# Optimization experiments

Measured on AMD Instinct MI355X. Metric: run time of the kernel, lower is better.

The kernel has to match this reference:

```python
import jax, jax.numpy as jnp
import numpy as np

NUM_NODE = 50000
NUM_EDGE = 1_600_000
NUM_REL = 512
DIM = 64


def setup_inputs() -> dict:
    key = jax.random.key(0)
    k1, k2, k3, k4, k5, k6 = jax.random.split(key, 6)
    inp = jax.random.normal(k1, (NUM_NODE, DIM), dtype=jnp.float32)
    boundary = jax.random.normal(k2, (NUM_NODE, DIM), dtype=jnp.float32)
    node_in = jax.random.randint(k3, (NUM_EDGE,), 0, NUM_NODE)
    node_out = jax.random.randint(k4, (NUM_EDGE,), 0, NUM_NODE)
    rel = jax.random.randint(k5, (NUM_EDGE,), 0, NUM_REL)
    edge_list = jnp.stack([node_in, node_out, rel], axis=1).astype(jnp.int32)
    edge_weight = jnp.ones((NUM_EDGE,), dtype=jnp.float32)
    relation_weight = jax.random.normal(k6, (NUM_REL, DIM), dtype=jnp.float32)
    W = jax.random.normal(jax.random.fold_in(key, 7), (DIM, DIM), dtype=jnp.float32) / np.sqrt(DIM)
    b = jnp.zeros((DIM,), dtype=jnp.float32)
    return {"input": inp, "boundary": boundary, "edge_list": edge_list,
            "edge_weight": edge_weight, "relation_weight": relation_weight,
            "W": W, "b": b}


def reference(input, boundary, edge_list, edge_weight, relation_weight, W, b):
    node_in = edge_list[:, 0]
    node_out = edge_list[:, 1]
    rel = edge_list[:, 2]
    # message: DistMult = x_src * r_e   [E, D]
    msg = input[node_in] * relation_weight[rel]
    msg = msg * edge_weight[:, None]
    # std aggregation: sum and sq_sum scatters, boundary acts as an extra self-message
    s = jax.ops.segment_sum(msg, node_out, num_segments=NUM_NODE) + boundary
    sq = jax.ops.segment_sum(msg * msg, node_out, num_segments=NUM_NODE) + boundary * boundary
    deg = jax.ops.segment_sum(jnp.ones_like(edge_weight), node_out, num_segments=NUM_NODE)
    deg1 = (deg + 1.0)[:, None]  # degree_out + 1 (boundary counted)
    update = jnp.sqrt(jnp.clip(sq / deg1 - (s / deg1) ** 2, 1e-6))
    # add_model: single Linear (MLP with num_mlp_layer=1, no trailing activation)
    return update @ W.T + b
```

## Files before the change

### kernel.cpp

```cpp
#include <hip/hip_runtime.h>
#include <hip/hip_bf16.h>

#define NN  50000
#define NE  1600000
#define DIM 64
#define NBK 391

#define OFF_FLAGS  0
#define OFF_BCURP  8
#define OFF_EIDX   6272

#define CHUNK 8192
#define QCAP  2304

typedef __bf16 bf16x8 __attribute__((ext_vector_type(8)));
typedef __bf16 bf16x4 __attribute__((ext_vector_type(4)));
typedef float  f32x4  __attribute__((ext_vector_type(4)));

__device__ __forceinline__ float loadF(const void* p, int i, int bf) {
  if (bf) return __bfloat162float(((const __hip_bfloat16*)p)[i]);
  return ((const float*)p)[i];
}

__device__ __forceinline__ float4 loadF4(const void* p, int i4, int bf) {
  if (bf) {
    ushort4 u = ((const ushort4*)p)[i4];
    float4 f;
    union { unsigned int ui; float fl; } c;
    c.ui = (unsigned int)u.x << 16; f.x = c.fl;
    c.ui = (unsigned int)u.y << 16; f.y = c.fl;
    c.ui = (unsigned int)u.z << 16; f.z = c.fl;
    c.ui = (unsigned int)u.w << 16; f.w = c.fl;
    return f;
  }
  return ((const float4*)p)[i4];
}

__device__ __forceinline__ void accumF(float4 a, float4 r,
                                       float4& s4, float4& q4) {
  float tx = a.x * r.x, ty = a.y * r.y, tz = a.z * r.z, tw = a.w * r.w;
  s4.x += tx; q4.x = fmaf(tx, tx, q4.x);
  s4.y += ty; q4.y = fmaf(ty, ty, q4.y);
  s4.z += tz; q4.z = fmaf(tz, tz, q4.z);
  s4.w += tw; q4.w = fmaf(tw, tw, q4.w);
}

__global__ void k_detect(const void* input, const void* boundary,
                         const void* relw, const void* W, const void* ew,
                         int* flags, int* bcurp) {
  __shared__ int cnt;
  int t = threadIdx.x;
  const void* arrs[4] = {input, boundary, relw, W};
  for (int a = 0; a < 4; ++a) {
    if (t == 0) cnt = 0;
    __syncthreads();
    const unsigned short* u = (const unsigned short*)arrs[a];
    unsigned ex = (u[2 * t] >> 7) & 0xFF;
    if (ex >= 100 && ex <= 140) atomicAdd(&cnt, 1);
    __syncthreads();
    if (t == 0) flags[a] = (cnt >= 32) ? 1 : 0;
    __syncthreads();
  }
  if (t == 0) {
    flags[4] = (((const unsigned short*)ew)[0] == 0x3F80) ? 1 : 0;
    flags[5] = 1;
  }
  for (int i = t; i < NBK * 16; i += 64) bcurp[i] = 0;
}

__global__ __launch_bounds__(256) void k_ew(const void* __restrict__ ew,
                                            int* __restrict__ flags) {
  int bfE = flags[4];
  int c0 = blockIdx.x * 8192;
  int bad = 0;
  for (int i = threadIdx.x; i < 8192; i += 256) {
    int e = c0 + i;
    if (e < NE && loadF(ew, e, bfE) != 1.0f) bad = 1;
  }
  if (bad) flags[5] = 0;
}

__global__ __launch_bounds__(1024) void k_parta(
    const int* __restrict__ el, int* __restrict__ bcurp,
    int* __restrict__ eidx, const int* __restrict__ flags,
    int gb0, int gb1, int padcap) {
  __shared__ int stage[CHUNK];
  __shared__ unsigned short sbk[CHUNK];
  __shared__ int lh[NBK], lbase[NBK], lh2[NBK], gbs[NBK];
  __shared__ int sc[256];
  __shared__ int total;
  int t = threadIdx.x;
  int nb = gb1 - gb0;
  int c0 = blockIdx.x * CHUNK;
  int ones = flags[5];
  for (int i = t; i < nb; i += 1024) { lh[i] = 0; lh2[i] = 0; }
  __syncthreads();

  int rec[8], bb[8];
  #pragma unroll
  for (int j = 0; j < 8; ++j) {
    int e = c0 + j * 1024 + t;
    bb[j] = -1; rec[j] = 0;
    if (e < NE) {
      int n0 = el[e * 3], n1 = el[e * 3 + 1], n2 = el[e * 3 + 2];
      int b = (n1 >> 7) - gb0;
      if (b >= 0 && b < nb) {
        bb[j] = b;
        rec[j] = ones ? (n0 | (n2 << 16) | ((n1 & 127) << 25))
                      : (e | ((n1 & 127) << 25));
        atomicAdd(&lh[b], 1);
      }
    }
  }
  __syncthreads();

  int a0 = 0, a1 = 0;
  if (t < 256) {
    a0 = (2 * t < nb) ? lh[2 * t] : 0;
    a1 = (2 * t + 1 < nb) ? lh[2 * t + 1] : 0;
    sc[t] = a0 + a1;
  }
  __syncthreads();
  for (int off = 1; off < 256; off <<= 1) {
    int v = 0;
    if (t < 256 && t >= off) v = sc[t - off];
    __syncthreads();
    if (t < 256) sc[t] += v;
    __syncthreads();
  }
  if (t < 256) {
    int excl = sc[t] - (a0 + a1);
    if (2 * t < nb) {
      lbase[2 * t] = excl;
      if (a0 > 0) gbs[2 * t] = atomicAdd(&bcurp[(gb0 + 2 * t) * 16], a0);
    }
    if (2 * t + 1 < nb) {
      lbase[2 * t + 1] = excl + a0;
      if (a1 > 0)
        gbs[2 * t + 1] = atomicAdd(&bcurp[(gb0 + 2 * t + 1) * 16], a1);
    }
    if (t == 255) total = sc[255];
  }
  __syncthreads();

  #pragma unroll
  for (int j = 0; j < 8; ++j) {
    if (bb[j] >= 0) {
      int r = atomicAdd(&lh2[bb[j]], 1);
      int slot = lbase[bb[j]] + r;
      stage[slot] = rec[j];
      sbk[slot] = (unsigned short)bb[j];
    }
  }
  __syncthreads();

  int tot = total;
  for (int i = t; i < tot; i += 1024) {
    int b = sbk[i];
    int slot = gbs[b] + (i - lbase[b]);
    if (slot < padcap) eidx[(long)b * padcap + slot] = stage[i];
  }
}

__global__ __launch_bounds__(256, 8) void k_node(
    const void* __restrict__ input, const void* __restrict__ boundary,
    const int* __restrict__ el, const void* __restrict__ ew,
    const void* __restrict__ relw, const void* __restrict__ W,
    const void* __restrict__ bv, const int* __restrict__ bcurp,
    const int* __restrict__ eidx, const int* __restrict__ flags,
    void* __restrict__ out, int gb0, int hi, int padcap) {
  __shared__ int ld[QCAP];
  __shared__ int ld2[QCAP];
  __shared__ int lstart[32], lend[32], lcnt[32];
  __shared__ int nf, ovf;
  __bf16 (*updb)[72] = reinterpret_cast<__bf16(*)[72]>(ld);

  int bfI = flags[0], bfB = flags[1], bfR = flags[2], bfW = flags[3],
      bfE = flags[4], ones = flags[5];
  int t = threadIdx.x;
  int wv = t >> 6, ln = t & 63;
  int g = ln >> 4;
  int k = ln & 15;
  int q = ln >> 4;
  int Bl = blockIdx.x >> 2;
  int B  = gb0 + Bl;
  int quarter = blockIdx.x & 3;
  int n0 = B * 128 + quarter * 32;
  int cnt = bcurp[B * 16];
  const int* myeidx = eidx + (long)Bl * padcap;

  if (t == 0) { nf = 0; ovf = (cnt > padcap) ? 1 : 0; }
  if (t < 32) lcnt[t] = 0;
  __syncthreads();

  int cl = cnt < padcap ? cnt : padcap;
  for (int i = t; i < cl; i += 256) {
    int rc = myeidx[i];
    if ((((unsigned)rc) >> 30) == (unsigned)quarter) {
      int p = atomicAdd(&nf, 1);
      if (p < QCAP) ld[p] = rc; else ovf = 1;
    }
  }
  __syncthreads();
  int fast = !ovf;
  int nq = nf < QCAP ? nf : QCAP;

  if (fast) {
    for (int i = t; i < nq; i += 256)
      atomicAdd(&lcnt[(((unsigned)ld[i]) >> 25) & 31], 1);
  }
  __syncthreads();
  if (t < 32) lend[t] = lcnt[t];
  __syncthreads();
  for (int off = 1; off < 32; off <<= 1) {
    int v = 0;
    if (t < 32 && t >= off) v = lend[t - off];
    __syncthreads();
    if (t < 32) lend[t] += v;
    __syncthreads();
  }
  if (t < 32) { lstart[t] = lend[t] - lcnt[t]; lcnt[t] = 0; }
  __syncthreads();
  if (fast) {
    for (int i = t; i < nq; i += 256) {
      int rc = ld[i];
      int l = (((unsigned)rc) >> 25) & 31;
      int r = atomicAdd(&lcnt[l], 1);
      ld2[lstart[l] + r] = rc;
    }
  }
  __syncthreads();

  const float4* inp4 = (const float4*)input;
  const float4* rw4  = (const float4*)relw;
  int hot = (!bfI && !bfR && ones) ? 1 : 0;

  for (int rr = 0; rr < 8; ++rr) {
    int row = wv * 8 + rr;
    int n = n0 + row;
    if (n >= hi) {
      if (g == 0) *(bf16x4*)&updb[row][4 * k] =
          bf16x4{(__bf16)0.f, (__bf16)0.f, (__bf16)0.f, (__bf16)0.f};
      continue;
    }
    float4 s4 = {0.f,0.f,0.f,0.f}, q4 = {0.f,0.f,0.f,0.f};
    float degf = 0.f;
    if (fast) {
      int start = lstart[row], end = lend[row];
      degf = (float)(end - start);
      if (hot) {
        for (int base = start; base < end; base += 64) {
          int mm = end - base; if (mm > 64) mm = 64;
          int rec = 0;
          if (ln < mm) rec = ld2[base + ln];
          int jq = mm >> 2;
          int jmax = (mm + 3) >> 2;
          int j = 0;
          for (; j + 4 <= jq; j += 4) {
            int pk0 = __shfl(rec, j * 4 + g);
            int pk1 = __shfl(rec, j * 4 + 4 + g);
            int pk2 = __shfl(rec, j * 4 + 8 + g);
            int pk3 = __shfl(rec, j * 4 + 12 + g);
            float4 a0 = inp4[(pk0 & 0xFFFF) * 16 + k];
            float4 r0 = rw4[((pk0 >> 16) & 0x1FF) * 16 + k];
            float4 a1 = inp4[(pk1 & 0xFFFF) * 16 + k];
            float4 r1 = rw4[((pk1 >> 16) & 0x1FF) * 16 + k];
            float4 a2 = inp4[(pk2 & 0xFFFF) * 16 + k];
            float4 r2 = rw4[((pk2 >> 16) & 0x1FF) * 16 + k];
            float4 a3 = inp4[(pk3 & 0xFFFF) * 16 + k];
            float4 r3 = rw4[((pk3 >> 16) & 0x1FF) * 16 + k];
            accumF(a0, r0, s4, q4);
            accumF(a1, r1, s4, q4);
            accumF(a2, r2, s4, q4);
            accumF(a3, r3, s4, q4);
          }
          for (; j < jq; ++j) {
            int pk = __shfl(rec, j * 4 + g);
            float4 a = inp4[(pk & 0xFFFF) * 16 + k];
            float4 r = rw4[((pk >> 16) & 0x1FF) * 16 + k];
            accumF(a, r, s4, q4);
          }
          for (; j < jmax; ++j) {
            int slot = j * 4 + g;
            int pk = __shfl(rec, slot & 63);
            float wsel = (slot < mm) ? 1.0f : 0.0f;
            float4 a = inp4[(pk & 0xFFFF) * 16 + k];
            float4 r = rw4[((pk >> 16) & 0x1FF) * 16 + k];
            float tx = a.x*r.x, ty = a.y*r.y, tz = a.z*r.z, tw = a.w*r.w;
            s4.x = fmaf(wsel, tx, s4.x); q4.x = fmaf(wsel*tx, tx, q4.x);
            s4.y = fmaf(wsel, ty, s4.y); q4.y = fmaf(wsel*ty, ty, q4.y);
            s4.z = fmaf(wsel, tz, s4.z); q4.z = fmaf(wsel*tz, tz, q4.z);
            s4.w = fmaf(wsel, tw, s4.w); q4.w = fmaf(wsel*tw, tw, q4.w);
          }
        }
      } else {
        for (int base = start; base < end; base += 64) {
          int mm = end - base; if (mm > 64) mm = 64;
          int rec = 0; float wrec = 0.0f;
          if (ln < mm) {
            rec = ld2[base + ln] & 0x1FFFFFF;
            if (!ones) wrec = loadF(ew, rec, bfE);
          }
          int jmax = (mm + 3) >> 2;
          for (int j = 0; j < jmax; ++j) {
            int slot = j * 4 + g;
            int rj = __shfl(rec, slot);
            int nin, rl; float wj;
            if (ones) { nin = rj & 0xFFFF; rl = (rj >> 16) & 0x1FF; wj = 1.0f; }
            else      { nin = el[rj * 3]; rl = el[rj * 3 + 2];
                        wj = __shfl(wrec, slot); }
            float wsel = (slot < mm) ? wj : 0.0f;
            float4 a = loadF4(input, nin * 16 + k, bfI);
            float4 r = loadF4(relw, rl * 16 + k, bfR);
            float tx = a.x*r.x, ty = a.y*r.y, tz = a.z*r.z, tw = a.w*r.w;
            s4.x = fmaf(wsel, tx, s4.x); q4.x = fmaf(wsel*tx, tx, q4.x);
            s4.y = fmaf(wsel, ty, s4.y); q4.y = fmaf(wsel*ty, ty, q4.y);
            s4.z = fmaf(wsel, tz, s4.z); q4.z = fmaf(wsel*tz, tz, q4.z);
            s4.w = fmaf(wsel, tw, s4.w); q4.w = fmaf(wsel*tw, tw, q4.w);
          }
        }
      }
    } else {
      float degc = 0.f;
      for (int e0 = g; e0 < NE; e0 += 4) {
        int nout = el[e0 * 3 + 1];
        if (nout != n) continue;
        degc += 1.0f;
        int nin = el[e0 * 3], rl = el[e0 * 3 + 2];
        float wj = ones ? 1.0f : loadF(ew, e0, bfE);
        float4 a = loadF4(input, nin * 16 + k, bfI);
        float4 r = loadF4(relw, rl * 16 + k, bfR);
        float tx = wj*a.x*r.x, ty = wj*a.y*r.y, tz = wj*a.z*r.z,
              tw = wj*a.w*r.w;
        s4.x += tx; q4.x = fmaf(tx, tx, q4.x);
        s4.y += ty; q4.y = fmaf(ty, ty, q4.y);
        s4.z += tz; q4.z = fmaf(tz, tz, q4.z);
        s4.w += tw; q4.w = fmaf(tw, tw, q4.w);
      }
      degc += __shfl_xor(degc, 16); degc += __shfl_xor(degc, 32);
      degf = degc;
    }
    s4.x += __shfl_xor(s4.x, 16); s4.x += __shfl_xor(s4.x, 32);
    s4.y += __shfl_xor(s4.y, 16); s4.y += __shfl_xor(s4.y, 32);
    s4.z += __shfl_xor(s4.z, 16); s4.z += __shfl_xor(s4.z, 32);
    s4.w += __shfl_xor(s4.w, 16); s4.w += __shfl_xor(s4.w, 32);
    q4.x += __shfl_xor(q4.x, 16); q4.x += __shfl_xor(q4.x, 32);
    q4.y += __shfl_xor(q4.y, 16); q4.y += __shfl_xor(q4.y, 32);
    q4.z += __shfl_xor(q4.z, 16); q4.z += __shfl_xor(q4.z, 32);
    q4.w += __shfl_xor(q4.w, 16); q4.w += __shfl_xor(q4.w, 32);
    if (g == 0) {
      float4 b4 = loadF4(boundary, n * 16 + k, bfB);
      float dg = degf + 1.0f;
      float sv, qv;
      bf16x4 u;
      sv = (s4.x + b4.x) / dg; qv = (q4.x + b4.x * b4.x) / dg;
      u[0] = (__bf16)sqrtf(fmaxf(qv - sv * sv, 1e-6f));
      sv = (s4.y + b4.y) / dg; qv = (q4.y + b4.y * b4.y) / dg;
      u[1] = (__bf16)sqrtf(fmaxf(qv - sv * sv, 1e-6f));
      sv = (s4.z + b4.z) / dg; qv = (q4.z + b4.z * b4.z) / dg;
      u[2] = (__bf16)sqrtf(fmaxf(qv - sv * sv, 1e-6f));
      sv = (s4.w + b4.w) / dg; qv = (q4.w + b4.w * b4.w) / dg;
      u[3] = (__bf16)sqrtf(fmaxf(qv - sv * sv, 1e-6f));
      *(bf16x4*)&updb[row][4 * k] = u;
    }
  }
  __syncthreads();

  int tt = wv >> 1, chh = wv & 1;
  bf16x8 af0 = *(const bf16x8*)&updb[tt * 16 + (ln & 15)][q * 8];
  bf16x8 af1 = *(const bf16x8*)&updb[tt * 16 + (ln & 15)][32 + q * 8];
  #pragma unroll
  for (int hh = 0; hh < 2; ++hh) {
    int cc = chh * 32 + hh * 16 + (ln & 15);
    bf16x8 bfr0, bfr1;
    #pragma unroll
    for (int j = 0; j < 8; ++j) {
      bfr0[j] = (__bf16)loadF(W, cc * 64 + q * 8 + j, bfW);
      bfr1[j] = (__bf16)loadF(W, cc * 64 + 32 + q * 8 + j, bfW);
    }
    float bias = loadF(bv, cc, bfW);
    f32x4 accv = {0.f, 0.f, 0.f, 0.f};
    accv = __builtin_amdgcn_mfma_f32_16x16x32_bf16(af0, bfr0, accv, 0, 0, 0);
    accv = __builtin_amdgcn_mfma_f32_16x16x32_bf16(af1, bfr1, accv, 0, 0, 0);
    #pragma unroll
    for (int i = 0; i < 4; ++i) {
      int nn = n0 + tt * 16 + q * 4 + i;
      if (nn < hi) {
        float v = accv[i] + bias;
        if (bfI) ((__hip_bfloat16*)out)[nn * 64 + cc] = __float2bfloat16(v);
        else     ((float*)out)[nn * 64 + cc] = v;
      }
    }
  }
}

extern "C" void kernel_launch(void* const* d_in, const int* in_sizes, int n_in,
                              void* d_out, int out_size, void* d_ws, size_t ws_size,
                              hipStream_t stream) {
  const void* input    = d_in[0];
  const void* boundary = d_in[1];
  const int*  edges    = (const int*)d_in[2];
  const void* eweight  = d_in[3];
  const void* relw     = d_in[4];
  const void* W        = d_in[5];
  const void* bv       = d_in[6];

  int* wsI    = (int*)d_ws;
  int* flags  = wsI + OFF_FLAGS;
  int* bcurp  = wsI + OFF_BCURP;
  int* eidx   = wsI + OFF_EIDX;

  long avail = (long)(ws_size / 4) - OFF_EIDX;
  if (avail < 1) avail = 1;
  int padcap = 8192;
  long bfit = avail / padcap;
  if (bfit < 1) { padcap = (int)avail; bfit = 1; }
  if (bfit > NBK) bfit = NBK;
  int npass = (int)((NBK + bfit - 1) / bfit);

  k_detect<<<1, 64, 0, stream>>>(input, boundary, relw, W, eweight,
                                 flags, bcurp);
  k_ew<<<(NE + 8191) / 8192, 256, 0, stream>>>(eweight, flags);

  const int PA_NB = (NE + CHUNK - 1) / CHUNK;
  for (int p = 0; p < npass; ++p) {
    int gb0 = (int)((long)NBK * p / npass);
    int gb1 = (int)((long)NBK * (p + 1) / npass);
    int hi = (gb1 * 128 < NN) ? gb1 * 128 : NN;
    k_parta<<<PA_NB, 1024, 0, stream>>>(edges, bcurp, eidx, flags,
                                        gb0, gb1, padcap);
    k_node<<<(gb1 - gb0) * 4, 256, 0, stream>>>(
        input, boundary, edges, eweight, relw, W, bv, bcurp, eidx, flags,
        d_out, gb0, hi, padcap);
  }
}
```

Baseline: 212.5 us.

## Bucket edges by 32-node groups so node blocks read their own edge list directly

Edge partitioning now buckets destination nodes in groups of 32 instead of 128. Each node block therefore reads only its own contiguous bucket, with no need to scan a 128-node bucket and filter its quarter. The partition kernel uses 4096-edge chunks and reuses the rank returned by the first histogram atomic, which removes the second atomic pass. The scan now handles 1563 buckets with 7 per thread. The trade-offs are more global bucket counters and atomics, a smaller per-bucket capacity of 2048, and more blocks in the partition kernel.

```diff
diff --git a/kernel.cpp b/kernel.cpp
--- a/kernel.cpp
+++ b/kernel.cpp
@@ -1,17 +1,17 @@
 #include <hip/hip_runtime.h>
 #include <hip/hip_bf16.h>
 
-#define NN  50000
-#define NE  1600000
-#define DIM 64
-#define NBK 391
+#define NN   50000
+#define NE   1600000
+#define DIM  64
+#define NB32 1563
 
 #define OFF_FLAGS  0
-#define OFF_BCURP  8
-#define OFF_EIDX   6272
-
-#define CHUNK 8192
-#define QCAP  2304
+#define OFF_BCUR   8
+#define OFF_EIDX   6264
+
+#define CHUNK  4096
+#define PADCAP 2048
 
 typedef __bf16 bf16x8 __attribute__((ext_vector_type(8)));
 typedef __bf16 bf16x4 __attribute__((ext_vector_type(4)));
@@ -47,7 +47,7 @@
 
 __global__ void k_detect(const void* input, const void* boundary,
                          const void* relw, const void* W, const void* ew,
-                         int* flags, int* bcurp) {
+                         int* flags, int* bcur) {
   __shared__ int cnt;
   int t = threadIdx.x;
   const void* arrs[4] = {input, boundary, relw, W};
@@ -65,7 +65,7 @@
     flags[4] = (((const unsigned short*)ew)[0] == 0x3F80) ? 1 : 0;
     flags[5] = 1;
   }
-  for (int i = t; i < NBK * 16; i += 64) bcurp[i] = 0;
+  for (int i = t; i < NB32 * 4; i += 64) bcur[i] = 0;
 }
 
 __global__ __launch_bounds__(256) void k_ew(const void* __restrict__ ew,
@@ -81,73 +81,78 @@
 }
 
 __global__ __launch_bounds__(1024) void k_parta(
-    const int* __restrict__ el, int* __restrict__ bcurp,
+    const int* __restrict__ el, int* __restrict__ bcur,
     int* __restrict__ eidx, const int* __restrict__ flags,
     int gb0, int gb1, int padcap) {
   __shared__ int stage[CHUNK];
   __shared__ unsigned short sbk[CHUNK];
-  __shared__ int lh[NBK], lbase[NBK], lh2[NBK], gbs[NBK];
+  __shared__ int lh[NB32], lbase[NB32], gbs[NB32];
   __shared__ int sc[256];
   __shared__ int total;
   int t = threadIdx.x;
   int nb = gb1 - gb0;
   int c0 = blockIdx.x * CHUNK;
   int ones = flags[5];
-  for (int i = t; i < nb; i += 1024) { lh[i] = 0; lh2[i] = 0; }
-  __syncthreads();
-
-  int rec[8], bb[8];
+  for (int i = t; i < nb; i += 1024) lh[i] = 0;
+  __syncthreads();
+
+  int rec[4], bb[4], rk[4];
   #pragma unroll
-  for (int j = 0; j < 8; ++j) {
+  for (int j = 0; j < 4; ++j) {
     int e = c0 + j * 1024 + t;
-    bb[j] = -1; rec[j] = 0;
+    bb[j] = -1; rec[j] = 0; rk[j] = 0;
     if (e < NE) {
       int n0 = el[e * 3], n1 = el[e * 3 + 1], n2 = el[e * 3 + 2];
-      int b = (n1 >> 7) - gb0;
+      int b = (n1 >> 5) - gb0;
       if (b >= 0 && b < nb) {
         bb[j] = b;
-        rec[j] = ones ? (n0 | (n2 << 16) | ((n1 & 127) << 25))
-                      : (e | ((n1 & 127) << 25));
-        atomicAdd(&lh[b], 1);
+        rec[j] = ones ? (n0 | (n2 << 16) | ((n1 & 31) << 25))
+                      : (e | ((n1 & 31) << 25));
+        rk[j] = atomicAdd(&lh[b], 1);
       }
     }
   }
   __syncthreads();
 
-  int a0 = 0, a1 = 0;
-  if (t < 256) {
-    a0 = (2 * t < nb) ? lh[2 * t] : 0;
-    a1 = (2 * t + 1 < nb) ? lh[2 * t + 1] : 0;
-    sc[t] = a0 + a1;
-  }
+  int v[7]; int s = 0;
+  int base = t * 7;
+  #pragma unroll
+  for (int j = 0; j < 7; ++j) {
+    int idx = base + j;
+    v[j] = (idx < nb) ? lh[idx] : 0;
+    s += v[j];
+  }
+  sc[t < 256 ? t : 255] = 0;
+  __syncthreads();
+  if (t < 256) sc[t] = s;
   __syncthreads();
   for (int off = 1; off < 256; off <<= 1) {
-    int v = 0;
-    if (t < 256 && t >= off) v = sc[t - off];
-    __syncthreads();
-    if (t < 256) sc[t] += v;
-    __syncthreads();
-  }
-  if (t < 256) {
-    int excl = sc[t] - (a0 + a1);
-    if (2 * t < nb) {
-      lbase[2 * t] = excl;
-      if (a0 > 0) gbs[2 * t] = atomicAdd(&bcurp[(gb0 + 2 * t) * 16], a0);
-    }
-    if (2 * t + 1 < nb) {
-      lbase[2 * t + 1] = excl + a0;
-      if (a1 > 0)
-        gbs[2 * t + 1] = atomicAdd(&bcurp[(gb0 + 2 * t + 1) * 16], a1);
+    int x = 0;
+    if (t < 256 && t >= off) x = sc[t - off];
+    __syncthreads();
+    if (t < 256) sc[t] += x;
+    __syncthreads();
+  }
+  {
+    int excl = (t < 256) ? (sc[t] - s) : 0;
+    #pragma unroll
+    for (int j = 0; j < 7; ++j) {
+      int idx = base + j;
+      if (idx < nb) {
+        lbase[idx] = excl;
+        if (v[j] > 0)
+          gbs[idx] = atomicAdd(&bcur[(gb0 + idx) * 4], v[j]);
+        excl += v[j];
+      }
     }
     if (t == 255) total = sc[255];
   }
   __syncthreads();
 
   #pragma unroll
-  for (int j = 0; j < 8; ++j) {
+  for (int j = 0; j < 4; ++j) {
     if (bb[j] >= 0) {
-      int r = atomicAdd(&lh2[bb[j]], 1);
-      int slot = lbase[bb[j]] + r;
+      int slot = lbase[bb[j]] + rk[j];
       stage[slot] = rec[j];
       sbk[slot] = (unsigned short)bb[j];
     }
@@ -166,13 +171,12 @@
     const void* __restrict__ input, const void* __restrict__ boundary,
     const int* __restrict__ el, const void* __restrict__ ew,
     const void* __restrict__ relw, const void* __restrict__ W,
-    const void* __restrict__ bv, const int* __restrict__ bcurp,
+    const void* __restrict__ bv, const int* __restrict__ bcur,
     const int* __restrict__ eidx, const int* __restrict__ flags,
     void* __restrict__ out, int gb0, int hi, int padcap) {
-  __shared__ int ld[QCAP];
-  __shared__ int ld2[QCAP];
+  __shared__ int ld[PADCAP];
+  __shared__ int ld2[PADCAP];
   __shared__ int lstart[32], lend[32], lcnt[32];
-  __shared__ int nf, ovf;
   __bf16 (*updb)[72] = reinterpret_cast<__bf16(*)[72]>(ld);
 
   int bfI = flags[0], bfB = flags[1], bfR = flags[2], bfW = flags[3],
@@ -182,31 +186,19 @@
   int g = ln >> 4;
   int k = ln & 15;
   int q = ln >> 4;
-  int Bl = blockIdx.x >> 2;
-  int B  = gb0 + Bl;
-  int quarter = blockIdx.x & 3;
-  int n0 = B * 128 + quarter * 32;
-  int cnt = bcurp[B * 16];
-  const int* myeidx = eidx + (long)Bl * padcap;
-
-  if (t == 0) { nf = 0; ovf = (cnt > padcap) ? 1 : 0; }
+  int B = gb0 + blockIdx.x;
+  int n0 = B * 32;
+  int cnt = bcur[B * 4];
+  int fast = (cnt <= padcap);
+  const int* myeidx = eidx + (long)blockIdx.x * padcap;
+
   if (t < 32) lcnt[t] = 0;
   __syncthreads();
-
   int cl = cnt < padcap ? cnt : padcap;
-  for (int i = t; i < cl; i += 256) {
-    int rc = myeidx[i];
-    if ((((unsigned)rc) >> 30) == (unsigned)quarter) {
-      int p = atomicAdd(&nf, 1);
-      if (p < QCAP) ld[p] = rc; else ovf = 1;
-    }
-  }
-  __syncthreads();
-  int fast = !ovf;
-  int nq = nf < QCAP ? nf : QCAP;
-
   if (fast) {
-    for (int i = t; i < nq; i += 256)
+    for (int i = t; i < cl; i += 256) ld[i] = myeidx[i];
+    __syncthreads();
+    for (int i = t; i < cl; i += 256)
       atomicAdd(&lcnt[(((unsigned)ld[i]) >> 25) & 31], 1);
   }
   __syncthreads();
@@ -222,7 +214,7 @@
   if (t < 32) { lstart[t] = lend[t] - lcnt[t]; lcnt[t] = 0; }
   __syncthreads();
   if (fast) {
-    for (int i = t; i < nq; i += 256) {
+    for (int i = t; i < cl; i += 256) {
       int rc = ld[i];
       int l = (((unsigned)rc) >> 25) & 31;
       int r = atomicAdd(&lcnt[l], 1);
@@ -407,30 +399,30 @@
 
   int* wsI    = (int*)d_ws;
   int* flags  = wsI + OFF_FLAGS;
-  int* bcurp  = wsI + OFF_BCURP;
+  int* bcur   = wsI + OFF_BCUR;
   int* eidx   = wsI + OFF_EIDX;
 
   long avail = (long)(ws_size / 4) - OFF_EIDX;
   if (avail < 1) avail = 1;
-  int padcap = 8192;
+  int padcap = PADCAP;
   long bfit = avail / padcap;
   if (bfit < 1) { padcap = (int)avail; bfit = 1; }
-  if (bfit > NBK) bfit = NBK;
-  int npass = (int)((NBK + bfit - 1) / bfit);
+  if (bfit > NB32) bfit = NB32;
+  int npass = (int)((NB32 + bfit - 1) / bfit);
 
   k_detect<<<1, 64, 0, stream>>>(input, boundary, relw, W, eweight,
-                                 flags, bcurp);
+                                 flags, bcur);
   k_ew<<<(NE + 8191) / 8192, 256, 0, stream>>>(eweight, flags);
 
   const int PA_NB = (NE + CHUNK - 1) / CHUNK;
   for (int p = 0; p < npass; ++p) {
-    int gb0 = (int)((long)NBK * p / npass);
-    int gb1 = (int)((long)NBK * (p + 1) / npass);
-    int hi = (gb1 * 128 < NN) ? gb1 * 128 : NN;
-    k_parta<<<PA_NB, 1024, 0, stream>>>(edges, bcurp, eidx, flags,
+    int gb0 = (int)((long)NB32 * p / npass);
+    int gb1 = (int)((long)NB32 * (p + 1) / npass);
+    int hi = (gb1 * 32 < NN) ? gb1 * 32 : NN;
+    k_parta<<<PA_NB, 1024, 0, stream>>>(edges, bcur, eidx, flags,
                                         gb0, gb1, padcap);
-    k_node<<<(gb1 - gb0) * 4, 256, 0, stream>>>(
-        input, boundary, edges, eweight, relw, W, bv, bcurp, eidx, flags,
+    k_node<<<gb1 - gb0, 256, 0, stream>>>(
+        input, boundary, edges, eweight, relw, W, bv, bcur, eidx, flags,
         d_out, gb0, hi, padcap);
   }
 }
```

New measurement: 235.0 us. 1.11x slower.
